# Performance work log

Measured on AMD Instinct MI355X. Metric: run time of the kernel, lower is better.

Reference implementation:

```python
import jax, jax.numpy as jnp
import numpy as np

B, L = 4, 2048
D_Q = D_K = D_V = 512
D_MODEL = 512
H = 8  # heads; head dim = D_MODEL // H = 64


def _conv1x1(x, W, b):
    # Conv1d with kernel_size=1 == pointwise linear over channels.
    # x: (B, C_in, L), W: (C_out, C_in), b: (C_out,) -> (B, C_out, L)
    return jnp.einsum('oc,bcl->bol', W, x) + b[None, :, None]


def setup_inputs() -> dict:
    key = jax.random.key(0)
    ks = jax.random.split(key, 12)
    s = 0.02
    return {
        'q': jax.random.normal(ks[0], (B, D_Q, L), jnp.float32),
        'k': jax.random.normal(ks[1], (B, D_K, L), jnp.float32),
        'v': jax.random.normal(ks[2], (B, D_V, L), jnp.float32),
        'input_mask': jnp.ones((B, 1, L), jnp.float32),
        'Wq': jax.random.normal(ks[3], (D_MODEL, D_Q), jnp.float32) * s,
        'bq': jax.random.normal(ks[4], (D_MODEL,), jnp.float32) * s,
        'Wk': jax.random.normal(ks[5], (D_MODEL, D_K), jnp.float32) * s,
        'bk': jax.random.normal(ks[6], (D_MODEL,), jnp.float32) * s,
        'Wv': jax.random.normal(ks[7], (D_MODEL, D_V), jnp.float32) * s,
        'bv': jax.random.normal(ks[8], (D_MODEL,), jnp.float32) * s,
        'Wout': jax.random.normal(ks[9], (D_V, D_MODEL), jnp.float32) * s,
        'bout': jax.random.normal(ks[10], (D_V,), jnp.float32) * s,
    }


def reference(q, k, v, input_mask, Wq, bq, Wk, bk, Wv, bv, Wout, bout):
    Bq, _, Lq = q.shape
    qh = _conv1x1(q, Wq, bq).reshape(Bq, H, -1, Lq)  # (B,H,D,L)
    kh = _conv1x1(k, Wk, bk).reshape(Bq, H, -1, Lq)
    vh = _conv1x1(v, Wv, bv).reshape(Bq, H, -1, Lq)
    Dh = qh.shape[2]
    scale = 1.0 / jnp.sqrt(jnp.asarray(Dh, qh.dtype))
    scores = jnp.einsum('bhdl,bhdn->bhln', qh, kh) * scale  # (B,H,L,L)
    # total_mask = ~input_mask[:, 0:1, :].bool(); True -> masked keys
    pad = input_mask[:, 0:1, :] <= 0.5  # (B,1,L_k)
    scores = jnp.where(pad[:, None, :, :], jnp.asarray(-1e9, scores.dtype), scores)
    attn = jax.nn.softmax(scores, axis=-1)  # attn_dropout is None in module
    out = jnp.einsum('bhdn,bhln->bhdl', vh, attn).reshape(Bq, -1, Lq)  # (B,d_model,L)
    # self.dropout is identity at inference; final 1x1 conv projection
    return _conv1x1(out, Wout, bout)  # (B, d_v, L)
```

## Files before the change

### kernel.cpp

```cpp
#include <hip/hip_runtime.h>
#include <hip/hip_bf16.h>


#define BB  4
#define LL  2048
#define CC  512
#define HH  8
#define DHH 64

typedef __attribute__((ext_vector_type(8)))  short bf16x8;
typedef __attribute__((ext_vector_type(4)))  short bf16x4;
typedef __attribute__((ext_vector_type(16))) float f32x16;
typedef __attribute__((ext_vector_type(2)))  unsigned uint2v;
typedef __attribute__((ext_vector_type(4)))  unsigned uint4v;

using us = unsigned short;

#if __has_builtin(__builtin_amdgcn_exp2f)
#define EXP2(x) __builtin_amdgcn_exp2f(x)
#else
#define EXP2(x) __expf(0.6931471805599453f * (x))
#endif

__device__ __forceinline__ us f2bu(float x) {
    unsigned u = __float_as_uint(x);
    return (us)((u + 0x7FFFu + ((u >> 16) & 1u)) >> 16);
}
__device__ __forceinline__ unsigned pk2(float a, float b) {
    unsigned r;
    asm("v_cvt_pk_bf16_f32 %0, %1, %2" : "=v"(r) : "v"(a), "v"(b));
    return r;
}
__device__ __forceinline__ bf16x4 pk4(float a, float b, float c, float d) {
    uint2v u; u[0] = pk2(a, b); u[1] = pk2(c, d);
    return __builtin_bit_cast(bf16x4, u);
}

__device__ __forceinline__ void transpose_body(const float* __restrict__ X,
                                               us* __restrict__ Xt,
                                               int b, int c0, int n0, int t)
{
    __shared__ float T[64][65];

    const float* Xb = X + ((size_t)b * CC + c0) * LL + n0;
    #pragma unroll
    for (int i = 0; i < 4; ++i) {
        const int cl = (t >> 4) + 16 * i, nl = (t & 15) * 4;
        const float4 f = *(const float4*)(Xb + (size_t)cl * LL + nl);
        T[cl][nl + 0] = f.x; T[cl][nl + 1] = f.y;
        T[cl][nl + 2] = f.z; T[cl][nl + 3] = f.w;
    }
    __syncthreads();
    us* Ot = Xt + ((size_t)b * LL + n0) * CC + c0;
    #pragma unroll
    for (int i = 0; i < 2; ++i) {
        const int nl = (t >> 3) + 32 * i, cb = (t & 7) * 8;
        uint4v u;
        #pragma unroll
        for (int j = 0; j < 4; ++j)
            u[j] = pk2(T[cb + 2 * j][nl], T[cb + 2 * j + 1][nl]);
        *(bf16x8*)(Ot + (size_t)nl * CC + cb) = __builtin_bit_cast(bf16x8, u);
    }
}

__global__ __launch_bounds__(256) void transpose_cvt(const float* __restrict__ X,
                                                     us* __restrict__ Xt)
{
    transpose_body(X, Xt, blockIdx.z, blockIdx.y * 64, blockIdx.x * 64, threadIdx.x);
}

__global__ __launch_bounds__(256) void transpose_cvt3(
    const float* __restrict__ Xq, const float* __restrict__ Xk,
    const float* __restrict__ Xv,
    us* __restrict__ X0, us* __restrict__ X1, us* __restrict__ X2)
{
    const int z = blockIdx.z, which = z >> 2, b = z & 3;
    const float* X = which == 0 ? Xq : (which == 1 ? Xk : Xv);
    us* Xt = which == 0 ? X0 : (which == 1 ? X1 : X2);
    transpose_body(X, Xt, b, blockIdx.y * 64, blockIdx.x * 64, threadIdx.x);
}

__global__ __launch_bounds__(256) void cvt_w4(const float* __restrict__ W0,
                                              const float* __restrict__ W1,
                                              const float* __restrict__ W2,
                                              const float* __restrict__ W3,
                                              us* __restrict__ out)
{
    const float* Ws[4] = {W0, W1, W2, W3};
    const float* W = Ws[blockIdx.y];
    us* O = out + (size_t)blockIdx.y * (CC * CC);
    const int i = (blockIdx.x * 256 + threadIdx.x) * 8;
    const float4 f0 = *(const float4*)(W + i);
    const float4 f1 = *(const float4*)(W + i + 4);
    uint4v u;
    u[0] = pk2(f0.x, f0.y); u[1] = pk2(f0.z, f0.w);
    u[2] = pk2(f1.x, f1.y); u[3] = pk2(f1.z, f1.w);
    *(bf16x8*)(O + i) = __builtin_bit_cast(bf16x8, u);
}

__device__ __forceinline__ void proj_body(const us* __restrict__ Xb,
                                          const us* __restrict__ Wm,
                                          const float* __restrict__ bias,
                                          float scale, void* __restrict__ Yv,
                                          int b, int n0, int m0, int t, int mode)
{
    const int lane = t & 63, wave = t >> 6;
    const int quad2 = lane >> 5, l31 = lane & 31;
    const int wr = (wave >> 1) * 64, wc = (wave & 1) * 64;

    __shared__ __align__(16) char PS[66048];
    __shared__ float biasS[128];

    f32x16 acc[2][2];
    #pragma unroll
    for (int mi = 0; mi < 2; ++mi)
        #pragma unroll
        for (int ni = 0; ni < 2; ++ni)
            #pragma unroll
            for (int e = 0; e < 16; ++e) acc[mi][ni][e] = 0.f;

    if (t < 128) biasS[t] = bias[m0 + t];

    const int wrO = (t & 7) * 2064 + (t >> 3) * 16;
    const int rdA = quad2 * 2064 + (wr + l31) * 16;
    const int rdB = 16512 + quad2 * 2064 + (wc + l31) * 16;

    #pragma unroll
    for (int i = 0; i < 4; ++i) {
        const int r = i * 32 + (t >> 3), bk = t & 7;
        *(bf16x8*)(PS + wrO + i * 512) =
            *(const bf16x8*)(Wm + (size_t)r * CC + bk * 8);
        *(bf16x8*)(PS + 16512 + wrO + i * 512) =
            *(const bf16x8*)(Xb + (size_t)(n0 + r) * CC + bk * 8);
    }
    __syncthreads();

    for (int it = 0; it < CC / 64; ++it) {
        const int cur = it & 1, k1 = (it + 1) * 64;
        char* PB = PS + (cur ? 33024 : 0);
        char* PN = PS + (cur ? 0 : 33024);

        bf16x8 apre[4], bpre[4];
        if (it + 1 < CC / 64) {
            #pragma unroll
            for (int i = 0; i < 4; ++i) {
                const int r = i * 32 + (t >> 3), bk = t & 7;
                apre[i] = *(const bf16x8*)(Wm + (size_t)r * CC + k1 + bk * 8);
                bpre[i] = *(const bf16x8*)(Xb + (size_t)(n0 + r) * CC + k1 + bk * 8);
            }
        }

        __builtin_amdgcn_s_setprio(1);
        #pragma unroll
        for (int ks = 0; ks < 4; ++ks) {
            const bf16x8 af0 = *(const bf16x8*)(PB + rdA + ks * 4128);
            const bf16x8 af1 = *(const bf16x8*)(PB + rdA + ks * 4128 + 512);
            const bf16x8 bf0 = *(const bf16x8*)(PB + rdB + ks * 4128);
            const bf16x8 bf1 = *(const bf16x8*)(PB + rdB + ks * 4128 + 512);
            acc[0][0] = __builtin_amdgcn_mfma_f32_32x32x16_bf16(af0, bf0, acc[0][0], 0, 0, 0);
            acc[0][1] = __builtin_amdgcn_mfma_f32_32x32x16_bf16(af0, bf1, acc[0][1], 0, 0, 0);
            acc[1][0] = __builtin_amdgcn_mfma_f32_32x32x16_bf16(af1, bf0, acc[1][0], 0, 0, 0);
            acc[1][1] = __builtin_amdgcn_mfma_f32_32x32x16_bf16(af1, bf1, acc[1][1], 0, 0, 0);
        }
        __builtin_amdgcn_s_setprio(0);

        if (it + 1 < CC / 64) {
            #pragma unroll
            for (int i = 0; i < 4; ++i) {
                *(bf16x8*)(PN + wrO + i * 512) = apre[i];
                *(bf16x8*)(PN + 16512 + wrO + i * 512) = bpre[i];
            }
        }
        __syncthreads();
    }

    #pragma unroll
    for (int mi = 0; mi < 2; ++mi)
        #pragma unroll
        for (int ni = 0; ni < 2; ++ni) {
            const int nloc = wc + ni * 32 + l31;
            if (mode == 0) {
                us* Y = (us*)Yv;
                #pragma unroll
                for (int rg2 = 0; rg2 < 4; ++rg2) {
                    const int rbase = wr + mi * 32 + 8 * rg2 + 4 * quad2;
                    float v0 = (acc[mi][ni][rg2 * 4 + 0] + biasS[rbase + 0]) * scale;
                    float v1 = (acc[mi][ni][rg2 * 4 + 1] + biasS[rbase + 1]) * scale;
                    float v2 = (acc[mi][ni][rg2 * 4 + 2] + biasS[rbase + 2]) * scale;
                    float v3 = (acc[mi][ni][rg2 * 4 + 3] + biasS[rbase + 3]) * scale;
                    const int mg = m0 + rbase;
                    const int h = mg >> 6, d = mg & 63;
                    *(bf16x4*)(Y + (((size_t)(b * HH + h) * LL) + n0 + nloc) * DHH + d) =
                        pk4(v0, v1, v2, v3);
                }
            } else {
                #pragma unroll
                for (int reg = 0; reg < 16; ++reg) {
                    const int row = (reg & 3) + 8 * (reg >> 2) + 4 * quad2;
                    const int mloc = wr + mi * 32 + row;
                    const float v = (acc[mi][ni][reg] + biasS[mloc]) * scale;
                    const size_t addr = ((size_t)b * CC + m0 + mloc) * LL + n0 + nloc;
                    if (mode == 1) ((us*)Yv)[addr] = f2bu(v);
                    else           ((float*)Yv)[addr] = v;
                }
            }
        }
}

template <int MODE>
__global__ __launch_bounds__(256, 2) void proj_gemm(const us* __restrict__ Xt,
                                                    const us* __restrict__ Wb,
                                                    const float* __restrict__ bias,
                                                    float scale,
                                                    void* __restrict__ Yv)
{
    const int b = blockIdx.z, n0 = blockIdx.x * 128, m0 = blockIdx.y * 128;
    proj_body(Xt + (size_t)b * LL * CC, Wb + (size_t)m0 * CC, bias, scale, Yv,
              b, n0, m0, threadIdx.x, MODE);
}

__global__ __launch_bounds__(256, 2) void proj_gemm3(
    const us* __restrict__ X0, const us* __restrict__ X1, const us* __restrict__ X2,
    const us* __restrict__ Wb4,
    const float* __restrict__ bq, const float* __restrict__ bk,
    const float* __restrict__ bv, float scale_q,
    us* __restrict__ qh, us* __restrict__ kh, us* __restrict__ vh)
{
    const int z = blockIdx.z, which = z >> 2, b = z & 3;
    const int n0 = blockIdx.x * 128, m0 = blockIdx.y * 128;
    const us* Xt = which == 0 ? X0 : (which == 1 ? X1 : X2);
    const us* Wb = Wb4 + (size_t)which * (CC * CC);
    const float* bias = which == 0 ? bq : (which == 1 ? bk : bv);
    const float scale = which == 0 ? scale_q : 1.0f;
    us* Yv = which == 0 ? qh : (which == 1 ? kh : vh);
    const int mode = (which == 2) ? 1 : 0;
    proj_body(Xt + (size_t)b * LL * CC, Wb + (size_t)m0 * CC, bias, scale,
              (void*)Yv, b, n0, m0, threadIdx.x, mode);
}

__global__ __launch_bounds__(512, 4) void attn_fwd(
    const us* __restrict__ Qh,
    const us* __restrict__ Kh,
    const us* __restrict__ Vh,
    const float* __restrict__ mask,
    us* __restrict__ ctx)
{
    const int bh = blockIdx.x;
    const int b = bh >> 3, h = bh & 7;
    const int qb = blockIdx.y;
    const int t = threadIdx.x, lane = t & 63, wave = t >> 6;
    const int half = wave >> 2, wv = wave & 3;
    const int quad2 = lane >> 5, l31 = lane & 31;
    const int th = t & 255;
    const int qg = qb * 128 + wv * 32;

    __shared__ __align__(16) char SM[66560];
    __shared__ unsigned long long mwS[32];

    const float* mb = mask + (size_t)b * LL;
    #pragma unroll
    for (int i = 0; i < 4; ++i) {
        const int tile = wave * 4 + i;
        const unsigned long long bal = __ballot(mb[tile * 64 + lane] > 0.5f);
        if (lane == 0) mwS[tile] = bal;
    }

    const us* Qbase = Qh + (size_t)bh * LL * DHH;
    bf16x8 qf[4];
    #pragma unroll
    for (int ks = 0; ks < 4; ++ks)
        qf[ks] = *(const bf16x8*)(Qbase + (size_t)(qg + l31) * DHH + ks * 16 + quad2 * 8);

    f32x16 of[2];
    #pragma unroll
    for (int mt = 0; mt < 2; ++mt)
        #pragma unroll
        for (int e = 0; e < 16; ++e) of[mt][e] = 0.f;
    float l_run = 0.f;

    const us* Kbase = Kh + (size_t)bh * LL * DHH;
    const us* Vbase = Vh + ((size_t)b * CC + h * DHH) * LL;

    char* SH = SM + half * 33280;
    const int wrO = (th & 7) * 1040 + (th >> 3) * 16;
    const int rdO = quad2 * 1040 + l31 * 16;
    const int g0 = half * 16;

    #pragma unroll
    for (int i = 0; i < 2; ++i) {
        const int r = i * 32 + (th >> 3), bk = th & 7;
        *(bf16x8*)(SH + wrO + i * 512) =
            *(const bf16x8*)(Kbase + (size_t)(g0 * 64 + r) * DHH + bk * 8);
        *(bf16x8*)(SH + 8320 + wrO + i * 512) =
            *(const bf16x8*)(Vbase + (size_t)r * LL + g0 * 64 + bk * 8);
    }
    __syncthreads();

    f32x16 sf[2];
    #pragma unroll
    for (int mt = 0; mt < 2; ++mt)
        #pragma unroll
        for (int e = 0; e < 16; ++e) sf[mt][e] = 0.f;
    {
        const char* pK = SH + rdO;
        __builtin_amdgcn_s_setprio(1);
        #pragma unroll
        for (int ks = 0; ks < 4; ++ks)
            #pragma unroll
            for (int mt = 0; mt < 2; ++mt)
                sf[mt] = __builtin_amdgcn_mfma_f32_32x32x16_bf16(
                    *(const bf16x8*)(pK + ks * 2080 + mt * 512), qf[ks], sf[mt], 0, 0, 0);
        __builtin_amdgcn_s_setprio(0);
    }

    for (int itl = 0; itl < 16; ++itl) {
        const int cur = itl & 1;
        char* SB = SH + (cur ? 16640 : 0);
        char* SN = SH + (cur ? 0 : 16640);

        bf16x8 kpre[2], vpre[2];
        if (itl + 1 < 16) {
            const int n1 = (g0 + itl + 1) * 64;
            #pragma unroll
            for (int i = 0; i < 2; ++i) {
                const int r = i * 32 + (th >> 3), bk = th & 7;
                kpre[i] = *(const bf16x8*)(Kbase + (size_t)(n1 + r) * DHH + bk * 8);
                vpre[i] = *(const bf16x8*)(Vbase + (size_t)r * LL + n1 + bk * 8);
            }
        }

        const unsigned long long mw = mwS[g0 + itl];
        const bool masked = (mw != 0xFFFFFFFFFFFFFFFFull);
        float ps = 0.f;
        bf16x8 pfrag[4];
        #pragma unroll
        for (int mt = 0; mt < 2; ++mt) {
            float p[16];
            #pragma unroll
            for (int e = 0; e < 16; ++e) p[e] = EXP2(sf[mt][e]);
            if (masked) {
                #pragma unroll
                for (int e = 0; e < 16; ++e) {
                    const int row = 32 * mt + (e & 3) + 8 * (e >> 2) + 4 * quad2;
                    p[e] = ((mw >> row) & 1ull) ? p[e] : 0.f;
                }
            }
            const float s0 = (p[0] + p[1]) + (p[2] + p[3]);
            const float s1 = (p[4] + p[5]) + (p[6] + p[7]);
            const float s2 = (p[8] + p[9]) + (p[10] + p[11]);
            const float s3 = (p[12] + p[13]) + (p[14] + p[15]);
            ps += (s0 + s1) + (s2 + s3);
            #pragma unroll
            for (int g = 0; g < 2; ++g) {
                unsigned w0 = pk2(p[8 * g + 0], p[8 * g + 1]);
                unsigned w1 = pk2(p[8 * g + 2], p[8 * g + 3]);
                unsigned w2 = pk2(p[8 * g + 4], p[8 * g + 5]);
                unsigned w3 = pk2(p[8 * g + 6], p[8 * g + 7]);
                asm("v_permlane32_swap_b32 %0, %1" : "+v"(w0), "+v"(w2));
                asm("v_permlane32_swap_b32 %0, %1" : "+v"(w1), "+v"(w3));
                uint4v u; u[0] = w0; u[1] = w1; u[2] = w2; u[3] = w3;
                pfrag[2 * mt + g] = __builtin_bit_cast(bf16x8, u);
            }
        }
        ps += __shfl_xor(ps, 32, 64);
        l_run += ps;

        __builtin_amdgcn_s_setprio(1);
        #pragma unroll
        for (int ks = 0; ks < 4; ++ks)
            #pragma unroll
            for (int mt = 0; mt < 2; ++mt) {
                const bf16x8 vf = *(const bf16x8*)(SB + 8320 + rdO + ks * 2080 + mt * 512);
                of[mt] = __builtin_amdgcn_mfma_f32_32x32x16_bf16(vf, pfrag[ks], of[mt], 0, 0, 0);
            }
        __builtin_amdgcn_s_setprio(0);

        if (itl + 1 < 16) {
            #pragma unroll
            for (int i = 0; i < 2; ++i) {
                *(bf16x8*)(SN + wrO + i * 512) = kpre[i];
                *(bf16x8*)(SN + 8320 + wrO + i * 512) = vpre[i];
            }
        }
        __syncthreads();

        if (itl + 1 < 16) {
            #pragma unroll
            for (int mt = 0; mt < 2; ++mt)
                #pragma unroll
                for (int e = 0; e < 16; ++e) sf[mt][e] = 0.f;
            __builtin_amdgcn_s_setprio(1);
            #pragma unroll
            for (int ks = 0; ks < 4; ++ks)
                #pragma unroll
                for (int mt = 0; mt < 2; ++mt)
                    sf[mt] = __builtin_amdgcn_mfma_f32_32x32x16_bf16(
                        *(const bf16x8*)(SN + rdO + ks * 2080 + mt * 512), qf[ks], sf[mt], 0, 0, 0);
            __builtin_amdgcn_s_setprio(0);
        }
    }

    float4* OS = (float4*)SM;
    float*  LS = (float*)(SM + 32768);
    if (half == 1) {
        #pragma unroll
        for (int mt = 0; mt < 2; ++mt)
            #pragma unroll
            for (int r4 = 0; r4 < 4; ++r4) {
                float4 v;
                v.x = of[mt][r4 * 4 + 0]; v.y = of[mt][r4 * 4 + 1];
                v.z = of[mt][r4 * 4 + 2]; v.w = of[mt][r4 * 4 + 3];
                OS[(wv * 8 + mt * 4 + r4) * 64 + lane] = v;
            }
        LS[wv * 64 + lane] = l_run;
    }
    __syncthreads();
    if (half == 0) {
        l_run += LS[wv * 64 + lane];
        const float inv = 1.0f / l_run;
        us* Cb = ctx + (size_t)b * LL * CC;
        const int q = qg + l31;
        #pragma unroll
        for (int mt = 0; mt < 2; ++mt)
            #pragma unroll
            for (int r4 = 0; r4 < 4; ++r4) {
                const float4 v = OS[(wv * 8 + mt * 4 + r4) * 64 + lane];
                const int d = 32 * mt + 8 * r4 + 4 * quad2;
                *(bf16x4*)(Cb + (size_t)q * CC + h * DHH + d) =
                    pk4((of[mt][r4 * 4 + 0] + v.x) * inv,
                        (of[mt][r4 * 4 + 1] + v.y) * inv,
                        (of[mt][r4 * 4 + 2] + v.z) * inv,
                        (of[mt][r4 * 4 + 3] + v.w) * inv);
            }
    }
}

extern "C" void kernel_launch(void* const* d_in, const int* in_sizes, int n_in,
                              void* d_out, int out_size, void* d_ws, size_t ws_size,
                              hipStream_t stream)
{
    const float* q    = (const float*)d_in[0];
    const float* k    = (const float*)d_in[1];
    const float* v    = (const float*)d_in[2];
    const float* mask = (const float*)d_in[3];
    const float* Wq   = (const float*)d_in[4];
    const float* bq   = (const float*)d_in[5];
    const float* Wk   = (const float*)d_in[6];
    const float* bk   = (const float*)d_in[7];
    const float* Wv   = (const float*)d_in[8];
    const float* bv   = (const float*)d_in[9];
    const float* Wout = (const float*)d_in[10];
    const float* bout = (const float*)d_in[11];

    const size_t TSZ  = (size_t)BB * CC * LL;
    const size_t WSZ  = (size_t)4 * CC * CC;
    const float SCALE_Q = 0.125f * 1.4426950408889634f;

    const dim3 tb(256), gb(256);

    if (ws_size >= (6 * TSZ + WSZ) * sizeof(us)) {
        us* X0  = (us*)d_ws;
        us* X1  = X0 + TSZ;
        us* X2  = X1 + TSZ;
        us* qh  = X2 + TSZ;
        us* kh  = qh + TSZ;
        us* vh  = kh + TSZ;
        us* Wb  = vh + TSZ;
        us* ctx = X0;

        cvt_w4<<<dim3(CC * CC / 2048, 4), tb, 0, stream>>>(Wq, Wk, Wv, Wout, Wb);
        transpose_cvt3<<<dim3(LL / 64, CC / 64, 12), tb, 0, stream>>>(q, k, v, X0, X1, X2);
        proj_gemm3<<<dim3(LL / 128, CC / 128, 12), gb, 0, stream>>>(
            X0, X1, X2, Wb, bq, bk, bv, SCALE_Q, qh, kh, vh);
        attn_fwd<<<dim3(HH * BB, LL / 128), dim3(512), 0, stream>>>(qh, kh, vh, mask, ctx);
        proj_gemm<2><<<dim3(LL / 128, CC / 128, BB), gb, 0, stream>>>(
            ctx, Wb + 3 * (size_t)CC * CC, bout, 1.0f, d_out);
    } else {
        us* Xt  = (us*)d_ws;
        us* qh  = Xt + TSZ;
        us* kh  = qh + TSZ;
        us* vh  = kh + TSZ;
        us* Wb  = vh + TSZ;
        us* ctx = Xt;

        const dim3 tg(LL / 64, CC / 64, BB), gg(LL / 128, CC / 128, BB);

        cvt_w4<<<dim3(CC * CC / 2048, 4), tb, 0, stream>>>(Wq, Wk, Wv, Wout, Wb);
        transpose_cvt<<<tg, tb, 0, stream>>>(q, Xt);
        proj_gemm<0><<<gg, gb, 0, stream>>>(Xt, Wb + 0 * (size_t)CC * CC, bq, SCALE_Q, (void*)qh);
        transpose_cvt<<<tg, tb, 0, stream>>>(k, Xt);
        proj_gemm<0><<<gg, gb, 0, stream>>>(Xt, Wb + 1 * (size_t)CC * CC, bk, 1.0f, (void*)kh);
        transpose_cvt<<<tg, tb, 0, stream>>>(v, Xt);
        proj_gemm<1><<<gg, gb, 0, stream>>>(Xt, Wb + 2 * (size_t)CC * CC, bv, 1.0f, (void*)vh);
        attn_fwd<<<dim3(HH * BB, LL / 128), dim3(512), 0, stream>>>(qh, kh, vh, mask, ctx);
        proj_gemm<2><<<gg, gb, 0, stream>>>(ctx, Wb + 3 * (size_t)CC * CC, bout, 1.0f, d_out);
    }
}
```

Baseline: 204.8 us.

## Stage Q in shared memory and single-buffer V to cut register pressure

Q fragments are now staged once in LDS and reloaded each iteration instead of being held in registers, and the S=QK^T computation moves from after the barrier to the start of each iteration. V becomes single-buffered and K stays double-buffered, which needs a second barrier per iteration before V can be overwritten. The intent is to free VGPRs (qf and the carried sf) so occupancy improves. The cost is extra LDS reads, an extra sync per tile, and less overlap between the QK MFMAs and the loads.

```diff
diff --git a/kernel.cpp b/kernel.cpp
--- a/kernel.cpp
+++ b/kernel.cpp
@@ -252,10 +252,9 @@
     const int half = wave >> 2, wv = wave & 3;
     const int quad2 = lane >> 5, l31 = lane & 31;
     const int th = t & 255;
-    const int qg = qb * 128 + wv * 32;
 
     __shared__ __align__(16) char SM[66560];
-    __shared__ unsigned long long mwS[32];
+    unsigned long long* mwS = (unsigned long long*)(SM + 66304);
 
     const float* mb = mask + (size_t)b * LL;
     #pragma unroll
@@ -265,11 +264,31 @@
         if (lane == 0) mwS[tile] = bal;
     }
 
-    const us* Qbase = Qh + (size_t)bh * LL * DHH;
-    bf16x8 qf[4];
-    #pragma unroll
-    for (int ks = 0; ks < 4; ++ks)
-        qf[ks] = *(const bf16x8*)(Qbase + (size_t)(qg + l31) * DHH + ks * 16 + quad2 * 8);
+    const us* Qg = Qh + ((size_t)bh * LL + qb * 128) * DHH;
+    #pragma unroll
+    for (int i = 0; i < 2; ++i) {
+        const int c = t + i * 512, row = c & 127, bk = c >> 7;
+        *(bf16x8*)(SM + c * 16) = *(const bf16x8*)(Qg + row * DHH + bk * 8);
+    }
+
+    const us* Kbase = Kh + (size_t)bh * LL * DHH;
+    const us* Vbase = Vh + ((size_t)b * CC + h * DHH) * LL;
+    char* KH = SM + 16384 + half * 16640;
+    char* VH = SM + 49664 + half * 8320;
+    const int wrO = (th & 7) * 1040 + (th >> 3) * 16;
+    const int rdO = quad2 * 1040 + l31 * 16;
+    const int qrd = quad2 * 2048 + (wv * 32 + l31) * 16;
+    const int g0 = half * 16;
+
+    #pragma unroll
+    for (int i = 0; i < 2; ++i) {
+        const int r = i * 32 + (th >> 3), bk = th & 7;
+        *(bf16x8*)(KH + wrO + i * 512) =
+            *(const bf16x8*)(Kbase + (size_t)(g0 * 64 + r) * DHH + bk * 8);
+        *(bf16x8*)(VH + wrO + i * 512) =
+            *(const bf16x8*)(Vbase + (size_t)r * LL + g0 * 64 + bk * 8);
+    }
+    __syncthreads();
 
     f32x16 of[2];
     #pragma unroll
@@ -278,45 +297,10 @@
         for (int e = 0; e < 16; ++e) of[mt][e] = 0.f;
     float l_run = 0.f;
 
-    const us* Kbase = Kh + (size_t)bh * LL * DHH;
-    const us* Vbase = Vh + ((size_t)b * CC + h * DHH) * LL;
-
-    char* SH = SM + half * 33280;
-    const int wrO = (th & 7) * 1040 + (th >> 3) * 16;
-    const int rdO = quad2 * 1040 + l31 * 16;
-    const int g0 = half * 16;
-
-    #pragma unroll
-    for (int i = 0; i < 2; ++i) {
-        const int r = i * 32 + (th >> 3), bk = th & 7;
-        *(bf16x8*)(SH + wrO + i * 512) =
-            *(const bf16x8*)(Kbase + (size_t)(g0 * 64 + r) * DHH + bk * 8);
-        *(bf16x8*)(SH + 8320 + wrO + i * 512) =
-            *(const bf16x8*)(Vbase + (size_t)r * LL + g0 * 64 + bk * 8);
-    }
-    __syncthreads();
-
-    f32x16 sf[2];
-    #pragma unroll
-    for (int mt = 0; mt < 2; ++mt)
-        #pragma unroll
-        for (int e = 0; e < 16; ++e) sf[mt][e] = 0.f;
-    {
-        const char* pK = SH + rdO;
-        __builtin_amdgcn_s_setprio(1);
-        #pragma unroll
-        for (int ks = 0; ks < 4; ++ks)
-            #pragma unroll
-            for (int mt = 0; mt < 2; ++mt)
-                sf[mt] = __builtin_amdgcn_mfma_f32_32x32x16_bf16(
-                    *(const bf16x8*)(pK + ks * 2080 + mt * 512), qf[ks], sf[mt], 0, 0, 0);
-        __builtin_amdgcn_s_setprio(0);
-    }
-
     for (int itl = 0; itl < 16; ++itl) {
         const int cur = itl & 1;
-        char* SB = SH + (cur ? 16640 : 0);
-        char* SN = SH + (cur ? 0 : 16640);
+        char* Kc = KH + cur * 8320;
+        char* Ka = KH + (1 - cur) * 8320;
 
         bf16x8 kpre[2], vpre[2];
         if (itl + 1 < 16) {
@@ -328,6 +312,23 @@
                 vpre[i] = *(const bf16x8*)(Vbase + (size_t)r * LL + n1 + bk * 8);
             }
         }
+
+        f32x16 sf[2];
+        #pragma unroll
+        for (int mt = 0; mt < 2; ++mt)
+            #pragma unroll
+            for (int e = 0; e < 16; ++e) sf[mt][e] = 0.f;
+        __builtin_amdgcn_s_setprio(1);
+        #pragma unroll
+        for (int ks = 0; ks < 4; ++ks) {
+            const bf16x8 qk = *(const bf16x8*)(SM + qrd + ks * 4096);
+            #pragma unroll
+            for (int mt = 0; mt < 2; ++mt) {
+                const bf16x8 af = *(const bf16x8*)(Kc + rdO + ks * 2080 + mt * 512);
+                sf[mt] = __builtin_amdgcn_mfma_f32_32x32x16_bf16(af, qk, sf[mt], 0, 0, 0);
+            }
+        }
+        __builtin_amdgcn_s_setprio(0);
 
         const unsigned long long mw = mwS[g0 + itl];
         const bool masked = (mw != 0xFFFFFFFFFFFFFFFFull);
@@ -370,38 +371,28 @@
         for (int ks = 0; ks < 4; ++ks)
             #pragma unroll
             for (int mt = 0; mt < 2; ++mt) {
-                const bf16x8 vf = *(const bf16x8*)(SB + 8320 + rdO + ks * 2080 + mt * 512);
+                const bf16x8 vf = *(const bf16x8*)(VH + rdO + ks * 2080 + mt * 512);
                 of[mt] = __builtin_amdgcn_mfma_f32_32x32x16_bf16(vf, pfrag[ks], of[mt], 0, 0, 0);
             }
         __builtin_amdgcn_s_setprio(0);
 
         if (itl + 1 < 16) {
             #pragma unroll
-            for (int i = 0; i < 2; ++i) {
-                *(bf16x8*)(SN + wrO + i * 512) = kpre[i];
-                *(bf16x8*)(SN + 8320 + wrO + i * 512) = vpre[i];
-            }
+            for (int i = 0; i < 2; ++i)
+                *(bf16x8*)(Ka + wrO + i * 512) = kpre[i];
         }
         __syncthreads();
-
         if (itl + 1 < 16) {
             #pragma unroll
-            for (int mt = 0; mt < 2; ++mt)
-                #pragma unroll
-                for (int e = 0; e < 16; ++e) sf[mt][e] = 0.f;
-            __builtin_amdgcn_s_setprio(1);
-            #pragma unroll
-            for (int ks = 0; ks < 4; ++ks)
-                #pragma unroll
-                for (int mt = 0; mt < 2; ++mt)
-                    sf[mt] = __builtin_amdgcn_mfma_f32_32x32x16_bf16(
-                        *(const bf16x8*)(SN + rdO + ks * 2080 + mt * 512), qf[ks], sf[mt], 0, 0, 0);
-            __builtin_amdgcn_s_setprio(0);
-        }
+            for (int i = 0; i < 2; ++i)
+                *(bf16x8*)(VH + wrO + i * 512) = vpre[i];
+        }
+        __syncthreads();
     }
 
     float4* OS = (float4*)SM;
     float*  LS = (float*)(SM + 32768);
+    const int qg = qb * 128 + wv * 32;
     if (half == 1) {
         #pragma unroll
         for (int mt = 0; mt < 2; ++mt)
```

Result: faster. 192.9 us (-5.8%).
